# Optimization experiments

Hardware: AMD Instinct MI355X
Metric: run time of the kernel (lower is better)

Reference implementation:

```python
import jax, jax.numpy as jnp
import numpy as np
from jax import lax

DIM = 256
B = 2
EPS = 1e-5


def setup_inputs() -> dict:
    key = jax.random.key(0)
    ks = jax.random.split(key, 8)
    d = DIM
    s = 0.02
    return {
        "x": jax.random.normal(ks[0], (B, d, d, d), jnp.float32),
        "conv_w": jax.random.normal(ks[1], (d, 1, 7, 7), jnp.float32) * s,
        "conv_b": jax.random.normal(ks[2], (d,), jnp.float32) * s,
        "ln_g": jnp.ones((d,), jnp.float32),
        "ln_b": jnp.zeros((d,), jnp.float32),
        "w1": jax.random.normal(ks[3], (4 * d, d), jnp.float32) * s,
        "b1": jax.random.normal(ks[4], (4 * d,), jnp.float32) * s,
        "w2": jax.random.normal(ks[5], (d, 4 * d), jnp.float32) * s,
        "b2": jax.random.normal(ks[6], (d,), jnp.float32) * s,
    }


def reference(x, conv_w, conv_b, ln_g, ln_b, w1, b1, w2, b2):
    dim = x.shape[1]
    # depthwise 7x7 conv, padding=3, NCHW / OIHW (O=dim, I=1)
    y = lax.conv_general_dilated(
        x, conv_w, window_strides=(1, 1), padding=((3, 3), (3, 3)),
        feature_group_count=dim, dimension_numbers=("NCHW", "OIHW", "NCHW"))
    y = y + conv_b[None, :, None, None]
    # LayerNorm over LAST axis (W) -- faithful to the original (un-permuted) code
    mu = jnp.mean(y, axis=-1, keepdims=True)
    var = jnp.mean(jnp.square(y - mu), axis=-1, keepdims=True)
    y = (y - mu) * lax.rsqrt(var + EPS) * ln_g + ln_b
    # MLP over last axis: dim -> 4*dim -> dim, exact GELU (torch default)
    y = jax.nn.gelu(jnp.einsum("bchw,ow->bcho", y, w1) + b1, approximate=False)
    y = jnp.einsum("bcho,wo->bchw", y, w2) + b2
    # rearrange 'b h w c -> b c h w' == transpose (0,3,1,2), then residual
    return x + jnp.transpose(y, (0, 3, 1, 2))
```

## Files before the change

kernel.cpp:

```cpp
#include <hip/hip_runtime.h>
#include <hip/hip_bf16.h>
#include <math.h>

using short8 = __attribute__((ext_vector_type(8))) short;
using f32x4  = __attribute__((ext_vector_type(4))) float;

static __device__ __forceinline__ f32x4 mfma16(short8 a, short8 b, f32x4 c){
    return __builtin_amdgcn_mfma_f32_16x16x32_bf16(a, b, c, 0, 0, 0);
}

static __device__ __forceinline__ unsigned short bf16of(float f){
    unsigned int u = __float_as_uint(f);
    unsigned int lsb = (u >> 16) & 1u;
    u += 0x7fffu + lsb;
    return (unsigned short)(u >> 16);
}

static __device__ __forceinline__ unsigned short bf16h(float f){
    return (unsigned short)((__float_as_uint(f) + 0x8000u) >> 16);
}

static __device__ __forceinline__ float gelu_fast(float x){
    float e = __builtin_amdgcn_exp2f(-2.4554669596f * x);
    return x * __builtin_amdgcn_rcpf(1.0f + e);
}

__global__ __launch_bounds__(256) void prep_weights(
    const float* __restrict__ w1, const float* __restrict__ w2,
    unsigned short* __restrict__ w1p, unsigned short* __restrict__ w2p)
{
    int t = blockIdx.x * 256 + threadIdx.x;
    int lane = t & 63;
    if (t < 32768){
        int g = t;
        int ks  = (g >> 6) & 7;
        int n16 = g >> 9;
        int o = n16*16 + (lane & 15);
        int k = ks*32 + (lane >> 4)*8;
        const float* src = w1 + o*256 + k;
        unsigned short* dst = w1p + (size_t)g*8;
        #pragma unroll
        for (int j = 0; j < 8; ++j) dst[j] = bf16of(src[j]);
    } else {
        int g = t - 32768;
        int ksg = (g >> 6) & 31;
        int n16 = g >> 11;
        int n = n16*16 + (lane & 15);
        int k = ksg*32 + (lane >> 4)*8;
        const float* src = w2 + n*1024 + k;
        unsigned short* dst = w2p + (size_t)g*8;
        #pragma unroll
        for (int j = 0; j < 8; ++j) dst[j] = bf16of(src[j]);
    }
}

#define CH 16
#define XR (CH + 6)
#define XWV 66
#define XW 264

__global__ __launch_bounds__(256) void conv_ln_kernel(
    const float* __restrict__ x, const float* __restrict__ conv_w,
    const float* __restrict__ conv_b, const float* __restrict__ ln_g,
    const float* __restrict__ ln_b, unsigned short* __restrict__ ynormF)
{
    __shared__ float xt[XR * XW];
    __shared__ float yt[CH * 256];
    unsigned short* ytn = (unsigned short*)xt;

    const int tid = threadIdx.x;
    const int blk = blockIdx.x;
    const int ht = blk & 15;
    const int c  = (blk >> 4) & 255;
    const int b  = blk >> 12;
    const int h0 = ht * CH;

    const float* xplane = x + (((size_t)(b*256 + c)) << 16);

    for (int i = tid; i < XR*XWV; i += 256){
        int ir = i / XWV;
        int cc = i - ir*XWV;
        int gh = h0 - 3 + ir;
        float4 v = make_float4(0.f, 0.f, 0.f, 0.f);
        if ((unsigned)gh < 256u && (unsigned)(cc - 1) < 64u)
            v = *reinterpret_cast<const float4*>(xplane + gh*256 + (cc - 1)*4);
        *reinterpret_cast<float4*>(&xt[ir*XW + cc*4]) = v;
    }

    float cwr[49];
    #pragma unroll
    for (int i = 0; i < 49; ++i) cwr[i] = conv_w[c*49 + i];
    const float cb = conv_b[c];

    __syncthreads();

    const int wq = tid & 63;
    const int hs = tid >> 6;
    float acc[4][4] = {};

    #pragma unroll
    for (int d = 0; d < 10; ++d){
        int ir = hs*4 + d;
        float4 ra = *reinterpret_cast<const float4*>(&xt[ir*XW + wq*4]);
        float4 rb = *reinterpret_cast<const float4*>(&xt[ir*XW + wq*4 + 4]);
        float4 rc = *reinterpret_cast<const float4*>(&xt[ir*XW + wq*4 + 8]);
        float rr[12] = {ra.x, ra.y, ra.z, ra.w, rb.x, rb.y, rb.z, rb.w,
                        rc.x, rc.y, rc.z, rc.w};
        #pragma unroll
        for (int ro = 0; ro < 4; ++ro){
            int dh = d - ro;
            if (dh >= 0 && dh <= 6){
                #pragma unroll
                for (int dw = 0; dw < 7; ++dw){
                    float wv = cwr[dh*7 + dw];
                    #pragma unroll
                    for (int cc = 0; cc < 4; ++cc)
                        acc[ro][cc] = fmaf(rr[cc + dw + 1], wv, acc[ro][cc]);
                }
            }
        }
    }

    #pragma unroll
    for (int ro = 0; ro < 4; ++ro){
        float4 v = make_float4(acc[ro][0] + cb, acc[ro][1] + cb,
                               acc[ro][2] + cb, acc[ro][3] + cb);
        *reinterpret_cast<float4*>(&yt[(hs*4 + ro)*256 + wq*4]) = v;
    }

    __syncthreads();

    const int lane = tid & 63;
    const int wid  = tid >> 6;
    float lg[4], lb[4];
    #pragma unroll
    for (int q = 0; q < 4; ++q){ lg[q] = ln_g[lane + 64*q]; lb[q] = ln_b[lane + 64*q]; }

    for (int rr2 = 0; rr2 < CH/4; ++rr2){
        int row = wid*(CH/4) + rr2;
        float v[4], s = 0.f, ss = 0.f;
        #pragma unroll
        for (int q = 0; q < 4; ++q){
            v[q] = yt[row*256 + lane + 64*q];
            s += v[q]; ss += v[q]*v[q];
        }
        #pragma unroll
        for (int off = 32; off > 0; off >>= 1){
            s  += __shfl_xor(s, off);
            ss += __shfl_xor(ss, off);
        }
        float mu  = s * (1.f/256.f);
        float var = ss * (1.f/256.f) - mu*mu;
        float rs  = rsqrtf(var + 1e-5f);
        #pragma unroll
        for (int q = 0; q < 4; ++q){
            float o = (v[q] - mu)*rs*lg[q] + lb[q];
            ytn[row*264 + lane + 64*q] = bf16of(o);
        }
    }

    __syncthreads();

    {
        const int l   = tid & 63;
        const int wv  = tid >> 6;
        const int l15w = l & 15, kgw = l >> 4;
        const int tile = (((b*256 + c)*256 + h0) >> 6);
        const int mf = (h0 >> 4) & 3;
        uint4* dst = reinterpret_cast<uint4*>(ynormF) + (size_t)tile*2048;
        #pragma unroll
        for (int it = 0; it < 2; ++it){
            int ks = wv*2 + it;
            uint4 v = *reinterpret_cast<const uint4*>(ytn + l15w*264 + ks*32 + kgw*8);
            dst[(ks*4 + mf)*64 + l] = v;
        }
    }
}

__global__ __launch_bounds__(256, 2) void mlp_kernel(
    const unsigned short* __restrict__ ynormF,
    const short* __restrict__ w1p, const short* __restrict__ w2p,
    const float* __restrict__ b1, const float* __restrict__ b2,
    const float* __restrict__ x, float* __restrict__ out)
{
    __shared__ __align__(16) char smem[65536];
    short* Ash = (short*)smem;
    short* Hs0 = (short*)(smem + 32768);
    short* Hs1 = (short*)(smem + 49152);

    const int tid  = threadIdx.x;
    const int lane = tid & 63;
    const int wid  = tid >> 6;
    const int tile = blockIdx.x;
    const int M0 = tile * 64;
    const int b = M0 >> 16, c = (M0 >> 8) & 255, h0 = M0 & 255;

    const int l15  = lane & 15;
    const int kg   = lane >> 4;

    {
        const uint4* src = reinterpret_cast<const uint4*>(ynormF) + (size_t)tile*2048;
        uint4* dst = reinterpret_cast<uint4*>(Ash);
        for (int i = tid; i < 2048; i += 256) dst[i] = src[i];
    }
    __syncthreads();

    f32x4 acc2[4][4];
    #pragma unroll
    for (int nfi = 0; nfi < 4; ++nfi){
        float4 bv = *reinterpret_cast<const float4*>(b2 + (wid*4 + nfi)*16 + kg*4);
        f32x4 b4 = {bv.x, bv.y, bv.z, bv.w};
        #pragma unroll
        for (int mf = 0; mf < 4; ++mf) acc2[mf][nfi] = b4;
    }

    f32x4 accA[4][2], accB[4][2];
    short8 pw2[4];

    auto gemm1 = [&](int oc, f32x4 (&acc1)[4][2]){
        #pragma unroll
        for (int nfi = 0; nfi < 2; ++nfi){
            float bb = b1[oc*128 + (wid*2 + nfi)*16 + l15];
            f32x4 bi = {bb, bb, bb, bb};
            #pragma unroll
            for (int mf = 0; mf < 4; ++mf) acc1[mf][nfi] = bi;
        }
        #pragma unroll
        for (int ks = 0; ks < 8; ++ks){
            short8 afr[4], bfr[2];
            #pragma unroll
            for (int mf = 0; mf < 4; ++mf)
                afr[mf] = *reinterpret_cast<const short8*>(
                    Ash + ((ks*4 + mf)*64 + lane)*8);
            #pragma unroll
            for (int nfi = 0; nfi < 2; ++nfi)
                bfr[nfi] = *reinterpret_cast<const short8*>(
                    w1p + ((size_t)(((oc*8 + wid*2 + nfi)*8 + ks)*64 + lane)) * 8);
            #pragma unroll
            for (int mf = 0; mf < 4; ++mf)
                #pragma unroll
                for (int nfi = 0; nfi < 2; ++nfi)
                    acc1[mf][nfi] = mfma16(afr[mf], bfr[nfi], acc1[mf][nfi]);
        }
    };

    auto gelu_store = [&](f32x4 (&acc1)[4][2], short* Hb){
        #pragma unroll
        for (int nfi = 0; nfi < 2; ++nfi){
            int col = (wid*2 + nfi)*16 + l15;
            #pragma unroll
            for (int mf = 0; mf < 4; ++mf){
                #pragma unroll
                for (int r = 0; r < 4; ++r){
                    int row = mf*16 + kg*4 + r;
                    Hb[row*128 + ((((col >> 3) ^ (row & 7))) << 3) + (col & 7)]
                        = (short)bf16h(gelu_fast(acc1[mf][nfi][r]));
                }
            }
        }
    };

    auto prefetch_pw2 = [&](int oc){
        #pragma unroll
        for (int nfi = 0; nfi < 4; ++nfi)
            pw2[nfi] = *reinterpret_cast<const short8*>(
                w2p + ((size_t)(((wid*4 + nfi)*32 + oc*4 + 0)*64 + lane)) * 8);
    };

    auto gemm2f = [&](int oc, short* Hb){
        #pragma unroll
        for (int ks = 0; ks < 4; ++ks){
            short8 hfr[4], wfr[4];
            #pragma unroll
            for (int mf = 0; mf < 4; ++mf){
                int row = mf*16 + l15;
                hfr[mf] = *reinterpret_cast<const short8*>(
                    Hb + row*128 + (((ks*4 + kg) ^ (l15 & 7)) << 3));
            }
            if (ks == 0){
                #pragma unroll
                for (int nfi = 0; nfi < 4; ++nfi) wfr[nfi] = pw2[nfi];
            } else {
                #pragma unroll
                for (int nfi = 0; nfi < 4; ++nfi)
                    wfr[nfi] = *reinterpret_cast<const short8*>(
                        w2p + ((size_t)(((wid*4 + nfi)*32 + oc*4 + ks)*64 + lane)) * 8);
            }
            #pragma unroll
            for (int mf = 0; mf < 4; ++mf)
                #pragma unroll
                for (int nfi = 0; nfi < 4; ++nfi)
                    acc2[mf][nfi] = mfma16(wfr[nfi], hfr[mf], acc2[mf][nfi]);
        }
    };

    gemm1(0, accA);
    gelu_store(accA, Hs0);
    gemm1(1, accB);
    prefetch_pw2(0);
    __syncthreads();

    #pragma unroll
    for (int oc = 0; oc < 8; ++oc){
        short* Hcur = (oc & 1) ? Hs1 : Hs0;
        gemm2f(oc, Hcur);
        if (oc < 7){
            f32x4 (&accR)[4][2] = ((oc + 1) & 1) ? accB : accA;
            gelu_store(accR, (oc & 1) ? Hs0 : Hs1);
        }
        if (oc < 6){
            f32x4 (&accW)[4][2] = ((oc + 2) & 1) ? accB : accA;
            gemm1(oc + 2, accW);
        }
        if (oc < 7){
            prefetch_pw2(oc + 1);
            __syncthreads();
        }
    }

    #pragma unroll
    for (int nfi = 0; nfi < 4; ++nfi){
        #pragma unroll
        for (int r = 0; r < 4; ++r){
            int w = (wid*4 + nfi)*16 + kg*4 + r;
            size_t base = ((size_t)b << 24) + ((size_t)w << 16) + (c << 8) + h0 + l15;
            #pragma unroll
            for (int mf = 0; mf < 4; ++mf){
                size_t o = base + mf*16;
                out[o] = acc2[mf][nfi][r] + x[o];
            }
        }
    }
}

extern "C" void kernel_launch(void* const* d_in, const int* in_sizes, int n_in,
                              void* d_out, int out_size, void* d_ws, size_t ws_size,
                              hipStream_t stream)
{
    const float* x      = (const float*)d_in[0];
    const float* conv_w = (const float*)d_in[1];
    const float* conv_b = (const float*)d_in[2];
    const float* ln_g   = (const float*)d_in[3];
    const float* ln_b   = (const float*)d_in[4];
    const float* w1     = (const float*)d_in[5];
    const float* b1     = (const float*)d_in[6];
    const float* w2     = (const float*)d_in[7];
    const float* b2     = (const float*)d_in[8];
    float* out = (float*)d_out;

    unsigned short* ynormF = (unsigned short*)d_ws;
    unsigned short* w1p    = (unsigned short*)((char*)d_ws + 67108864);
    unsigned short* w2p    = (unsigned short*)((char*)d_ws + 67108864 + 524288);

    hipLaunchKernelGGL(prep_weights, dim3(256), dim3(256), 0, stream, w1, w2, w1p, w2p);
    hipLaunchKernelGGL(conv_ln_kernel, dim3(8192), dim3(256), 0, stream,
                       x, conv_w, conv_b, ln_g, ln_b, ynormF);
    hipLaunchKernelGGL(mlp_kernel, dim3(2048), dim3(256), 0, stream,
                       ynormF, (const short*)w1p, (const short*)w2p, b1, b2, x, out);
}
```

Before: 254.5 us.

## Fuse LayerNorm into conv registers and hold MLP A-tile in registers

The conv+LN kernel now computes LayerNorm statistics straight from the per-thread conv accumulators with a wave shuffle reduction, dropping the fp32 staging tile and one barrier. It writes packed bf16 pairs to a dedicated LDS buffer. The MLP kernel loads its whole 64x256 bf16 A tile into registers instead of LDS, which cuts LDS to the two H buffers (32 KB). It also replaces the two-deep GEMM1 accumulator pipeline and the W2 prefetch with a single accumulator set. This trades LDS traffic and footprint for far more VGPRs (128 for A alone), which may spill or lower occupancy, and it loses the overlap the old software pipeline provided.

```diff
diff --git a/kernel.cpp b/kernel.cpp
--- a/kernel.cpp
+++ b/kernel.cpp
@@ -65,8 +65,7 @@
     const float* __restrict__ ln_b, unsigned short* __restrict__ ynormF)
 {
     __shared__ float xt[XR * XW];
-    __shared__ float yt[CH * 256];
-    unsigned short* ytn = (unsigned short*)xt;
+    __shared__ unsigned short ytn[CH * 264];
 
     const int tid = threadIdx.x;
     const int blk = blockIdx.x;
@@ -122,28 +121,21 @@
     }
 
     #pragma unroll
+    for (int ro = 0; ro < 4; ++ro)
+        #pragma unroll
+        for (int cc = 0; cc < 4; ++cc)
+            acc[ro][cc] += cb;
+
+    const float4 lgv = *reinterpret_cast<const float4*>(ln_g + wq*4);
+    const float4 lbv = *reinterpret_cast<const float4*>(ln_b + wq*4);
+    const float lg[4] = {lgv.x, lgv.y, lgv.z, lgv.w};
+    const float lb[4] = {lbv.x, lbv.y, lbv.z, lbv.w};
+
+    #pragma unroll
     for (int ro = 0; ro < 4; ++ro){
-        float4 v = make_float4(acc[ro][0] + cb, acc[ro][1] + cb,
-                               acc[ro][2] + cb, acc[ro][3] + cb);
-        *reinterpret_cast<float4*>(&yt[(hs*4 + ro)*256 + wq*4]) = v;
-    }
-
-    __syncthreads();
-
-    const int lane = tid & 63;
-    const int wid  = tid >> 6;
-    float lg[4], lb[4];
-    #pragma unroll
-    for (int q = 0; q < 4; ++q){ lg[q] = ln_g[lane + 64*q]; lb[q] = ln_b[lane + 64*q]; }
-
-    for (int rr2 = 0; rr2 < CH/4; ++rr2){
-        int row = wid*(CH/4) + rr2;
-        float v[4], s = 0.f, ss = 0.f;
-        #pragma unroll
-        for (int q = 0; q < 4; ++q){
-            v[q] = yt[row*256 + lane + 64*q];
-            s += v[q]; ss += v[q]*v[q];
-        }
+        float s  = acc[ro][0] + acc[ro][1] + acc[ro][2] + acc[ro][3];
+        float ss = acc[ro][0]*acc[ro][0] + acc[ro][1]*acc[ro][1]
+                 + acc[ro][2]*acc[ro][2] + acc[ro][3]*acc[ro][3];
         #pragma unroll
         for (int off = 32; off > 0; off >>= 1){
             s  += __shfl_xor(s, off);
@@ -152,11 +144,17 @@
         float mu  = s * (1.f/256.f);
         float var = ss * (1.f/256.f) - mu*mu;
         float rs  = rsqrtf(var + 1e-5f);
-        #pragma unroll
-        for (int q = 0; q < 4; ++q){
-            float o = (v[q] - mu)*rs*lg[q] + lb[q];
-            ytn[row*264 + lane + 64*q] = bf16of(o);
-        }
+        unsigned int u01, u23;
+        {
+            float o0 = (acc[ro][0] - mu)*rs*lg[0] + lb[0];
+            float o1 = (acc[ro][1] - mu)*rs*lg[1] + lb[1];
+            float o2 = (acc[ro][2] - mu)*rs*lg[2] + lb[2];
+            float o3 = (acc[ro][3] - mu)*rs*lg[3] + lb[3];
+            u01 = (unsigned int)bf16of(o0) | ((unsigned int)bf16of(o1) << 16);
+            u23 = (unsigned int)bf16of(o2) | ((unsigned int)bf16of(o3) << 16);
+        }
+        uint2 pv; pv.x = u01; pv.y = u23;
+        *reinterpret_cast<uint2*>(&ytn[(hs*4 + ro)*264 + wq*4]) = pv;
     }
 
     __syncthreads();
@@ -183,10 +181,7 @@
     const float* __restrict__ b1, const float* __restrict__ b2,
     const float* __restrict__ x, float* __restrict__ out)
 {
-    __shared__ __align__(16) char smem[65536];
-    short* Ash = (short*)smem;
-    short* Hs0 = (short*)(smem + 32768);
-    short* Hs1 = (short*)(smem + 49152);
+    __shared__ __align__(16) short Hs[2][64*128];
 
     const int tid  = threadIdx.x;
     const int lane = tid & 63;
@@ -198,12 +193,15 @@
     const int l15  = lane & 15;
     const int kg   = lane >> 4;
 
+    short8 Ar[8][4];
     {
-        const uint4* src = reinterpret_cast<const uint4*>(ynormF) + (size_t)tile*2048;
-        uint4* dst = reinterpret_cast<uint4*>(Ash);
-        for (int i = tid; i < 2048; i += 256) dst[i] = src[i];
-    }
-    __syncthreads();
+        const short8* asrc = reinterpret_cast<const short8*>(ynormF) + (size_t)tile*2048;
+        #pragma unroll
+        for (int ks = 0; ks < 8; ++ks)
+            #pragma unroll
+            for (int mf = 0; mf < 4; ++mf)
+                Ar[ks][mf] = asrc[(ks*4 + mf)*64 + lane];
+    }
 
     f32x4 acc2[4][4];
     #pragma unroll
@@ -214,10 +212,9 @@
         for (int mf = 0; mf < 4; ++mf) acc2[mf][nfi] = b4;
     }
 
-    f32x4 accA[4][2], accB[4][2];
-    short8 pw2[4];
-
-    auto gemm1 = [&](int oc, f32x4 (&acc1)[4][2]){
+    f32x4 acc1[4][2];
+
+    auto gemm1 = [&](int oc){
         #pragma unroll
         for (int nfi = 0; nfi < 2; ++nfi){
             float bb = b1[oc*128 + (wid*2 + nfi)*16 + l15];
@@ -227,24 +224,18 @@
         }
         #pragma unroll
         for (int ks = 0; ks < 8; ++ks){
-            short8 afr[4], bfr[2];
-            #pragma unroll
-            for (int mf = 0; mf < 4; ++mf)
-                afr[mf] = *reinterpret_cast<const short8*>(
-                    Ash + ((ks*4 + mf)*64 + lane)*8);
-            #pragma unroll
-            for (int nfi = 0; nfi < 2; ++nfi)
-                bfr[nfi] = *reinterpret_cast<const short8*>(
+            #pragma unroll
+            for (int nfi = 0; nfi < 2; ++nfi){
+                short8 bfr = *reinterpret_cast<const short8*>(
                     w1p + ((size_t)(((oc*8 + wid*2 + nfi)*8 + ks)*64 + lane)) * 8);
-            #pragma unroll
-            for (int mf = 0; mf < 4; ++mf)
                 #pragma unroll
-                for (int nfi = 0; nfi < 2; ++nfi)
-                    acc1[mf][nfi] = mfma16(afr[mf], bfr[nfi], acc1[mf][nfi]);
+                for (int mf = 0; mf < 4; ++mf)
+                    acc1[mf][nfi] = mfma16(Ar[ks][mf], bfr, acc1[mf][nfi]);
+            }
         }
     };
 
-    auto gelu_store = [&](f32x4 (&acc1)[4][2], short* Hb){
+    auto gelu_store = [&](short* Hb){
         #pragma unroll
         for (int nfi = 0; nfi < 2; ++nfi){
             int col = (wid*2 + nfi)*16 + l15;
@@ -260,60 +251,37 @@
         }
     };
 
-    auto prefetch_pw2 = [&](int oc){
-        #pragma unroll
-        for (int nfi = 0; nfi < 4; ++nfi)
-            pw2[nfi] = *reinterpret_cast<const short8*>(
-                w2p + ((size_t)(((wid*4 + nfi)*32 + oc*4 + 0)*64 + lane)) * 8);
-    };
-
-    auto gemm2f = [&](int oc, short* Hb){
+    auto gemm2f = [&](int oc, const short* Hb){
         #pragma unroll
         for (int ks = 0; ks < 4; ++ks){
-            short8 hfr[4], wfr[4];
+            short8 hfr[4];
             #pragma unroll
             for (int mf = 0; mf < 4; ++mf){
                 int row = mf*16 + l15;
                 hfr[mf] = *reinterpret_cast<const short8*>(
                     Hb + row*128 + (((ks*4 + kg) ^ (l15 & 7)) << 3));
             }
-            if (ks == 0){
+            #pragma unroll
+            for (int nfi = 0; nfi < 4; ++nfi){
+                short8 wfr = *reinterpret_cast<const short8*>(
+                    w2p + ((size_t)(((wid*4 + nfi)*32 + oc*4 + ks)*64 + lane)) * 8);
                 #pragma unroll
-                for (int nfi = 0; nfi < 4; ++nfi) wfr[nfi] = pw2[nfi];
-            } else {
-                #pragma unroll
-                for (int nfi = 0; nfi < 4; ++nfi)
-                    wfr[nfi] = *reinterpret_cast<const short8*>(
-                        w2p + ((size_t)(((wid*4 + nfi)*32 + oc*4 + ks)*64 + lane)) * 8);
-            }
-            #pragma unroll
-            for (int mf = 0; mf < 4; ++mf)
-                #pragma unroll
-                for (int nfi = 0; nfi < 4; ++nfi)
-                    acc2[mf][nfi] = mfma16(wfr[nfi], hfr[mf], acc2[mf][nfi]);
+                for (int mf = 0; mf < 4; ++mf)
+                    acc2[mf][nfi] = mfma16(wfr, hfr[mf], acc2[mf][nfi]);
+            }
         }
     };
 
-    gemm1(0, accA);
-    gelu_store(accA, Hs0);
-    gemm1(1, accB);
-    prefetch_pw2(0);
+    gemm1(0);
+    gelu_store(Hs[0]);
     __syncthreads();
 
     #pragma unroll
     for (int oc = 0; oc < 8; ++oc){
-        short* Hcur = (oc & 1) ? Hs1 : Hs0;
-        gemm2f(oc, Hcur);
+        if (oc < 7) gemm1(oc + 1);
+        gemm2f(oc, Hs[oc & 1]);
         if (oc < 7){
-            f32x4 (&accR)[4][2] = ((oc + 1) & 1) ? accB : accA;
-            gelu_store(accR, (oc & 1) ? Hs0 : Hs1);
-        }
-        if (oc < 6){
-            f32x4 (&accW)[4][2] = ((oc + 2) & 1) ? accB : accA;
-            gemm1(oc + 2, accW);
-        }
-        if (oc < 7){
-            prefetch_pw2(oc + 1);
+            gelu_store(Hs[(oc + 1) & 1]);
             __syncthreads();
         }
     }
```

Result: slower. 547.5 us (+115.1%).
